# Kernel tuning notes

Measured on AMD Instinct MI355X. Metric: run time of the kernel, lower is better.

Reference implementation:

```python
import jax, jax.numpy as jnp
import numpy as np

B, T, C = 2, 2048, 2048
H, H_KV, D = 32, 8, 64
ROPE_THETA = 10000.0


def _rope_cos_sin(t, head_dim, theta=ROPE_THETA):
    # t: [T] positions. Returns interleaved cos/sin of shape [T, head_dim]
    inv_freq = 1.0 / theta ** (jnp.arange(0, head_dim, 2, dtype=jnp.float32) / head_dim)
    freqs = jnp.outer(t.astype(jnp.float32), inv_freq)  # [T, D/2]
    cos = jnp.stack([jnp.cos(freqs), jnp.cos(freqs)], axis=-1).reshape(t.shape[0], head_dim)
    sin = jnp.stack([jnp.sin(freqs), jnp.sin(freqs)], axis=-1).reshape(t.shape[0], head_dim)
    return cos[None, None], sin[None, None]  # [1,1,T,D]


def _rotate_half(x):
    half = x.shape[-1] // 2
    return jnp.concatenate([-x[..., half:], x[..., :half]], axis=-1)


def setup_inputs() -> dict:
    key = jax.random.key(0)
    ks = jax.random.split(key, 5)
    std = 0.02
    return {
        "x": jax.random.normal(ks[0], (B, T, C), dtype=jnp.float32),
        "Wq": jax.random.normal(ks[1], (H * D, C), dtype=jnp.float32) * std,
        "Wk": jax.random.normal(ks[2], (H_KV * D, C), dtype=jnp.float32) * std,
        "Wv": jax.random.normal(ks[3], (H_KV * D, C), dtype=jnp.float32) * std,
        "Wc": jax.random.normal(ks[4], (C, C), dtype=jnp.float32) * std,
        "position_ids": jnp.arange(T, dtype=jnp.int32)[None, :],  # [1, T]
    }


def reference(x, Wq, Wk, Wv, Wc, position_ids):
    b, t, c = x.shape
    # QKV projections (torch Linear: y = x @ W.T)
    q = (x @ Wq.T).reshape(b, t, H, D).transpose(0, 2, 1, 3)       # [B,H,T,D]
    k = (x @ Wk.T).reshape(b, t, H_KV, D).transpose(0, 2, 1, 3)    # [B,Hkv,T,D]
    v = (x @ Wv.T).reshape(b, t, H_KV, D).transpose(0, 2, 1, 3)
    # GQA expand: repeat_interleave along head dim
    rep = H // H_KV
    k = jnp.repeat(k, rep, axis=1)  # [B,H,T,D]
    v = jnp.repeat(v, rep, axis=1)
    # RoPE (single-batch branch: interleaved cos/sin)
    cos, sin = _rope_cos_sin(position_ids[0], D)
    q = q * cos + _rotate_half(q) * sin
    k = k * cos + _rotate_half(k) * sin
    # causal SDPA
    scale = 1.0 / jnp.sqrt(jnp.asarray(D, dtype=q.dtype))
    scores = jnp.einsum("bhqd,bhkd->bhqk", q, k) * scale
    causal = jnp.tril(jnp.ones((t, t), dtype=bool))
    scores = jnp.where(causal[None, None], scores, jnp.finfo(scores.dtype).min)
    attn = jax.nn.softmax(scores, axis=-1)
    y = jnp.einsum("bhqk,bhkd->bhqd", attn, v)  # [B,H,T,D]
    y = y.transpose(0, 2, 1, 3).reshape(b, t, c)
    return y @ Wc.T
```

## Files before the change

kernel.cpp:

```cpp
#include <hip/hip_runtime.h>

constexpr int B   = 2;
constexpr int T   = 2048;
constexpr int C   = 2048;
constexpr int H   = 32;
constexpr int HKV = 8;
constexpr int D   = 64;
constexpr float SCALE = 0.125f;

typedef __attribute__((ext_vector_type(8))) short bf16x8;
typedef __attribute__((ext_vector_type(4))) float f32x4;

__device__ __forceinline__ unsigned short f2bf(float f) {
    unsigned u = __builtin_bit_cast(unsigned, f);
    u += 0x7fff + ((u >> 16) & 1);
    return (unsigned short)(u >> 16);
}
__device__ __forceinline__ float bf2f(unsigned short u) {
    unsigned v = (unsigned)u << 16;
    return __builtin_bit_cast(float, v);
}
__device__ __forceinline__ unsigned cvt_pk_bf16(float lo, float hi) {
    unsigned r;
    asm("v_cvt_pk_bf16_f32 %0, %1, %2" : "=v"(r) : "v"(lo), "v"(hi));
    return r;
}

typedef __attribute__((address_space(1))) const unsigned char ga_t;
typedef __attribute__((address_space(3))) unsigned char lds_t;
__device__ __forceinline__ void gl2lds16(const void* g, void* l) {
    __builtin_amdgcn_global_load_lds((ga_t*)g, (lds_t*)l, 16, 0, 0);
}

__global__ __launch_bounds__(256) void cast_all_bf16(const float* __restrict__ x,
                                                     const float* __restrict__ wq,
                                                     const float* __restrict__ wk,
                                                     const float* __restrict__ wv,
                                                     const float* __restrict__ wc,
                                                     unsigned short* __restrict__ out) {
    const size_t b0 = (size_t)B * T * C;
    const size_t b1 = b0 + (size_t)H * D * C;
    const size_t b2 = b1 + (size_t)HKV * D * C;
    const size_t b3 = b2 + (size_t)HKV * D * C;
    size_t i = ((size_t)blockIdx.x * 256 + threadIdx.x) * 8;
    const float* src;
    size_t off;
    if (i < b0)      { src = x;  off = i; }
    else if (i < b1) { src = wq; off = i - b0; }
    else if (i < b2) { src = wk; off = i - b1; }
    else if (i < b3) { src = wv; off = i - b2; }
    else             { src = wc; off = i - b3; }
    float4 a = *(const float4*)(src + off);
    float4 b = *(const float4*)(src + off + 4);
    uint4 r;
    r.x = (unsigned)f2bf(a.x) | ((unsigned)f2bf(a.y) << 16);
    r.y = (unsigned)f2bf(a.z) | ((unsigned)f2bf(a.w) << 16);
    r.z = (unsigned)f2bf(b.x) | ((unsigned)f2bf(b.y) << 16);
    r.w = (unsigned)f2bf(b.z) | ((unsigned)f2bf(b.w) << 16);
    *(uint4*)(out + i) = r;
}

template <typename OutT>
__device__ __forceinline__ void gemm_mfma_body(const unsigned short* __restrict__ Xh,
                                               const unsigned short* __restrict__ Wh,
                                               OutT* __restrict__ Y,
                                               int Nloc, int K, int bm, int bn) {
    __shared__ __align__(16) unsigned short As[128 * 32];
    __shared__ __align__(16) unsigned short Bs[128 * 32];
    char* AsB = (char*)As;
    char* BsB = (char*)Bs;

    const int tid  = threadIdx.x;
    const int wave = tid >> 6, lane = tid & 63;
    const int wm = (wave >> 1) * 64, wn = (wave & 1) * 64;
    const int m = lane & 15, quad = lane >> 4;

    const int r0 = tid >> 2;
    const int cs = tid & 3;
    const int cg = cs ^ (r0 & 3);
    const int wbase = (tid & 192) * 16;

    const unsigned short* gA = Xh + (size_t)(bm + r0) * K + cg * 8;
    const unsigned short* gB = Wh + (size_t)(bn + r0) * K + cg * 8;
    const size_t rowStep64 = (size_t)64 * K;

    int aoff[4], boff[4];
#pragma unroll
    for (int mt = 0; mt < 4; ++mt) {
        int ra = wm + mt * 16 + m;
        aoff[mt] = ra * 64 + ((quad ^ (ra & 3)) * 16);
        int rb = wn + mt * 16 + m;
        boff[mt] = rb * 64 + ((quad ^ (rb & 3)) * 16);
    }

    f32x4 acc[4][4];
#pragma unroll
    for (int i = 0; i < 4; ++i)
#pragma unroll
        for (int j = 0; j < 4; ++j) acc[i][j] = (f32x4){0.f, 0.f, 0.f, 0.f};

    for (int k0 = 0; k0 < K; k0 += 32) {
        gl2lds16(gA,             AsB + wbase);
        gl2lds16(gA + rowStep64, AsB + 4096 + wbase);
        gl2lds16(gB,             BsB + wbase);
        gl2lds16(gB + rowStep64, BsB + 4096 + wbase);
        gA += 32;
        gB += 32;
        __syncthreads();

        bf16x8 af[4], bfr[4];
#pragma unroll
        for (int mt = 0; mt < 4; ++mt) af[mt]  = *(const bf16x8*)(AsB + aoff[mt]);
#pragma unroll
        for (int nt = 0; nt < 4; ++nt) bfr[nt] = *(const bf16x8*)(BsB + boff[nt]);
#pragma unroll
        for (int mt = 0; mt < 4; ++mt)
#pragma unroll
            for (int nt = 0; nt < 4; ++nt)
                acc[mt][nt] = __builtin_amdgcn_mfma_f32_16x16x32_bf16(af[mt], bfr[nt],
                                                                      acc[mt][nt], 0, 0, 0);
        __syncthreads();
    }

#pragma unroll
    for (int mt = 0; mt < 4; ++mt)
#pragma unroll
        for (int r = 0; r < 4; ++r) {
            size_t row = (size_t)(bm + wm + mt * 16 + quad * 4 + r);
#pragma unroll
            for (int nt = 0; nt < 4; ++nt) {
                int col = bn + wn + nt * 16 + m;
                float v = acc[mt][nt][r];
                if constexpr (sizeof(OutT) == 2)
                    Y[row * Nloc + col] = f2bf(v);
                else
                    Y[row * Nloc + col] = v;
            }
        }
}

__global__ __launch_bounds__(256) void qkv_gemm_bf16(const unsigned short* __restrict__ Xh,
                                                     const unsigned short* __restrict__ Wqh,
                                                     const unsigned short* __restrict__ Wkh,
                                                     const unsigned short* __restrict__ Wvh,
                                                     unsigned short* __restrict__ qh,
                                                     unsigned short* __restrict__ kh,
                                                     unsigned short* __restrict__ vh) {
    int bn0 = blockIdx.x * 128;
    const unsigned short* Wsel;
    unsigned short* Ysel;
    int bnl, Nloc;
    if (bn0 < H * D)                { Wsel = Wqh; Ysel = qh; bnl = bn0;                  Nloc = H * D;   }
    else if (bn0 < H*D + HKV*D)     { Wsel = Wkh; Ysel = kh; bnl = bn0 - H * D;          Nloc = HKV * D; }
    else                            { Wsel = Wvh; Ysel = vh; bnl = bn0 - H*D - HKV*D;    Nloc = HKV * D; }
    gemm_mfma_body<unsigned short>(Xh, Wsel, Ysel, Nloc, C, blockIdx.y * 128, bnl);
}

__global__ __launch_bounds__(256) void out_gemm_bf16(const unsigned short* __restrict__ Xh,
                                                     const unsigned short* __restrict__ Wh,
                                                     float* __restrict__ Y) {
    gemm_mfma_body<float>(Xh, Wh, Y, C, C, blockIdx.y * 128, blockIdx.x * 128);
}

__global__ void rope_fused(unsigned short* __restrict__ qh, unsigned short* __restrict__ kh,
                           const int* __restrict__ pos_ids, float qscale) {
    int idx = blockIdx.x * blockDim.x + threadIdx.x;
    const int qtotal = B * T * H * 32;
    unsigned short* buf;
    int nheads, rel;
    float sc;
    if (idx < qtotal) { buf = qh; nheads = H;   sc = qscale; rel = idx; }
    else              { buf = kh; nheads = HKV; sc = 1.0f;   rel = idx - qtotal; }
    int d = rel & 31;
    int rest = rel >> 5;
    int t = (rest / nheads) % T;
    float pos = (float)pos_ids[t];
    int i1 = d >> 1;
    const float NEG_LF = -(2.0f / 64.0f) * 13.287712379549449f;
    float a1 = pos * exp2f(NEG_LF * (float)i1);
    float a2 = pos * exp2f(NEG_LF * (float)(i1 + 16));
    float c1 = cosf(a1), s1 = sinf(a1);
    float c2 = cosf(a2), s2 = sinf(a2);
    size_t base = (size_t)rest * D + d;
    float x1 = bf2f(buf[base]), x2 = bf2f(buf[base + 32]);
    buf[base]      = f2bf((x1 * c1 - x2 * s1) * sc);
    buf[base + 32] = f2bf((x2 * c2 + x1 * s2) * sc);
}

__global__ __launch_bounds__(256) void v_transpose(const unsigned short* __restrict__ vh,
                                                   unsigned short* __restrict__ vtg) {
    __shared__ unsigned short Vs[64][72];
    const int t0 = blockIdx.x * 64;
    const int hkv = blockIdx.y;
    const int b = blockIdx.z;
    const int tid = threadIdx.x;

    for (int e = tid; e < 512; e += 256) {
        int t = e >> 3, d8 = (e & 7) * 8;
        uint4 val = *(const uint4*)(vh + ((size_t)((b * T + t0 + t) * HKV) + hkv) * D + d8);
        unsigned short tmp[8];
        *(uint4*)tmp = val;
#pragma unroll
        for (int i = 0; i < 8; ++i) Vs[d8 + i][t] = tmp[i];
    }
    __syncthreads();
    for (int e = tid; e < 512; e += 256) {
        int d = e >> 3, c = e & 7;
        *(uint4*)(vtg + ((size_t)((b * HKV + hkv) * D) + d) * T + t0 + c * 8) =
            *(const uint4*)&Vs[d][c * 8];
    }
}

__global__ __launch_bounds__(256, 6) void flash_attn_mfma(const unsigned short* __restrict__ Qh,
                                                          const unsigned short* __restrict__ Kh,
                                                          const unsigned short* __restrict__ Vtg,
                                                          unsigned short* __restrict__ Yh) {
    __shared__ __align__(16) unsigned short Ks[64 * 64];
    __shared__ __align__(16) unsigned short Vt[64 * 64];
    __shared__ __align__(16) unsigned short Ps[4][16][72];

    const int q0 = ((int)gridDim.x - 1 - (int)blockIdx.x) * 64;
    const int h  = blockIdx.y;
    const int b  = blockIdx.z;
    const int hkv = h >> 2;
    const int tid = threadIdx.x;
    const int wave = tid >> 6;
    const int lane = tid & 63;
    const int m = lane & 15;
    const int quad = lane >> 4;

    const unsigned short* qrow = Qh + ((size_t)((b * T + q0 + wave * 16 + m) * H) + h) * D;
    const bf16x8 qa0 = *(const bf16x8*)(qrow + quad * 8);
    const bf16x8 qa1 = *(const bf16x8*)(qrow + 32 + quad * 8);

    f32x4 o[4];
#pragma unroll
    for (int dt = 0; dt < 4; ++dt) o[dt] = (f32x4){0.f, 0.f, 0.f, 0.f};
    float ms = -1e30f, ls = 0.f;

    const int r0 = tid >> 3, cs = tid & 7, cg = cs ^ (r0 & 7);
    const int wbase = (tid & 192) * 16;
    const unsigned short* gK = Kh + ((size_t)(b * T) * HKV + hkv) * D
                                  + (size_t)r0 * (HKV * D) + cg * 8;
    const unsigned short* gV = Vtg + ((size_t)(b * HKV + hkv) * D) * (size_t)T
                                   + (size_t)r0 * T + cg * 8;
    char* KsB = (char*)Ks;
    char* VtB = (char*)Vt;

    const int qmin = q0 + wave * 16;

    for (int k0 = 0; k0 <= q0; k0 += 64) {
        gl2lds16(gK,                          KsB + wbase);
        gl2lds16(gK + (size_t)32 * (HKV * D), KsB + 4096 + wbase);
        gl2lds16(gV,                          VtB + wbase);
        gl2lds16(gV + (size_t)32 * T,         VtB + 4096 + wbase);
        gK += (size_t)64 * (HKV * D);
        gV += 64;
        __syncthreads();

        f32x4 s[4];
        __builtin_amdgcn_s_setprio(1);
#pragma unroll
        for (int nt = 0; nt < 4; ++nt) {
            const int kmin = k0 + nt * 16;
            if (kmin > qmin + 15) {
                s[nt] = (f32x4){-1e30f, -1e30f, -1e30f, -1e30f};
                continue;
            }
            int row = nt * 16 + m;
            const bf16x8 ka0 = *(const bf16x8*)(KsB + row * 128 + ((quad ^ (m & 7)) * 16));
            const bf16x8 ka1 = *(const bf16x8*)(KsB + row * 128 + (((quad + 4) ^ (m & 7)) * 16));
            f32x4 acc = (f32x4){0.f, 0.f, 0.f, 0.f};
            acc = __builtin_amdgcn_mfma_f32_16x16x32_bf16(ka0, qa0, acc, 0, 0, 0);
            acc = __builtin_amdgcn_mfma_f32_16x16x32_bf16(ka1, qa1, acc, 0, 0, 0);
            if (kmin + 15 > qmin) {
                int c0 = qmin - kmin + m - 4 * quad;
#pragma unroll
                for (int r = 0; r < 4; ++r)
                    if (r > c0) acc[r] = -1e30f;
            }
            s[nt] = acc;
        }
        __builtin_amdgcn_s_setprio(0);

        float mx = s[0][0];
#pragma unroll
        for (int nt = 0; nt < 4; ++nt)
#pragma unroll
            for (int r = 0; r < 4; ++r) mx = fmaxf(mx, s[nt][r]);
        mx = fmaxf(mx, __shfl_xor(mx, 16));
        mx = fmaxf(mx, __shfl_xor(mx, 32));

        float al = 1.0f;
        if (__any(mx > ms + 8.0f)) {
            float mnew = fmaxf(ms, mx);
            al = exp2f(ms - mnew);
            ms = mnew;
            float av[4];
#pragma unroll
            for (int r = 0; r < 4; ++r)
                av[r] = __shfl(al, quad * 20 + r);
#pragma unroll
            for (int dt = 0; dt < 4; ++dt)
#pragma unroll
                for (int r = 0; r < 4; ++r) o[dt][r] *= av[r];
        }

        float psum = 0.f;
#pragma unroll
        for (int nt = 0; nt < 4; ++nt) {
            float p0 = exp2f(s[nt][0] - ms);
            float p1 = exp2f(s[nt][1] - ms);
            float p2 = exp2f(s[nt][2] - ms);
            float p3 = exp2f(s[nt][3] - ms);
            psum += (p0 + p1) + (p2 + p3);
            uint2 w;
            w.x = cvt_pk_bf16(p0, p1);
            w.y = cvt_pk_bf16(p2, p3);
            *(uint2*)&Ps[wave][m][nt * 16 + quad * 4] = w;
        }
        psum += __shfl_xor(psum, 16);
        psum += __shfl_xor(psum, 32);
        ls = ls * al + psum;

        const bf16x8 pa0 = *(const bf16x8*)&Ps[wave][m][quad * 8];
        const bf16x8 pa1 = *(const bf16x8*)&Ps[wave][m][32 + quad * 8];
        __builtin_amdgcn_s_setprio(1);
#pragma unroll
        for (int dt = 0; dt < 4; ++dt) {
            int vrow = dt * 16 + m;
            const bf16x8 vb0 = *(const bf16x8*)(VtB + vrow * 128 + ((quad ^ (m & 7)) * 16));
            const bf16x8 vb1 = *(const bf16x8*)(VtB + vrow * 128 + (((quad + 4) ^ (m & 7)) * 16));
            o[dt] = __builtin_amdgcn_mfma_f32_16x16x32_bf16(pa0, vb0, o[dt], 0, 0, 0);
            o[dt] = __builtin_amdgcn_mfma_f32_16x16x32_bf16(pa1, vb1, o[dt], 0, 0, 0);
        }
        __builtin_amdgcn_s_setprio(0);
        __syncthreads();
    }

#pragma unroll
    for (int r = 0; r < 4; ++r) {
        float lv = __shfl(ls, quad * 20 + r);
        float inv = 1.0f / lv;
        int trow = q0 + wave * 16 + quad * 4 + r;
        unsigned short* yp = Yh + ((size_t)(b * T + trow) * H + h) * D;
#pragma unroll
        for (int dt = 0; dt < 4; ++dt)
            yp[dt * 16 + m] = f2bf(o[dt][r] * inv);
    }
}

extern "C" void kernel_launch(void* const* d_in, const int* in_sizes, int n_in,
                              void* d_out, int out_size, void* d_ws, size_t ws_size,
                              hipStream_t stream) {
    const float* x  = (const float*)d_in[0];
    const float* Wq = (const float*)d_in[1];
    const float* Wk = (const float*)d_in[2];
    const float* Wv = (const float*)d_in[3];
    const float* Wc = (const float*)d_in[4];
    const int*  pos = (const int*)d_in[5];
    float* out = (float*)d_out;

    unsigned short* xh  = (unsigned short*)d_ws;
    unsigned short* wqh = xh  + (size_t)B * T * C;
    unsigned short* wkh = wqh + (size_t)H * D * C;
    unsigned short* wvh = wkh + (size_t)HKV * D * C;
    unsigned short* wch = wvh + (size_t)HKV * D * C;
    unsigned short* qh  = wch + (size_t)C * C;
    unsigned short* kh  = qh  + (size_t)B * T * H * D;
    unsigned short* vh  = kh  + (size_t)B * T * HKV * D;
    unsigned short* vtg = vh  + (size_t)B * T * HKV * D;
    unsigned short* yh  = xh;

    const size_t cast_total = (size_t)B * T * C + (size_t)(H + 2 * HKV) * D * C + (size_t)C * C;
    cast_all_bf16<<<(unsigned)(cast_total / (256 * 8)), 256, 0, stream>>>(x, Wq, Wk, Wv, Wc, xh);

    dim3 g1((H * D + 2 * HKV * D) / 128, (B * T) / 128);
    qkv_gemm_bf16<<<g1, 256, 0, stream>>>(xh, wqh, wkh, wvh, qh, kh, vh);

    const float QSCALE = SCALE * 1.4426950408889634f;
    rope_fused<<<(B * T * (H + HKV) * 32) / 256, 256, 0, stream>>>(qh, kh, pos, QSCALE);
    v_transpose<<<dim3(T / 64, HKV, B), 256, 0, stream>>>(vh, vtg);

    dim3 g2(T / 64, H, B);
    flash_attn_mfma<<<g2, 256, 0, stream>>>(qh, kh, vtg, yh);

    dim3 g3(C / 128, (B * T) / 128);
    out_gemm_bf16<<<g3, 256, 0, stream>>>(yh, wch, out);
}
```

Measured before the change: 376.7 us.

## Prefetch next K/V tile into registers to overlap global loads with compute

Replaces the direct global-to-LDS loads in the attention loop with register staging. The next K/V tile is loaded into registers while the current tile is being computed, then written to LDS at the start of the following iteration. The __syncthreads calls become explicit lgkmcnt waits plus s_barrier, so the barrier no longer waits on outstanding global loads. This hides global load latency at the cost of extra VGPRs and explicit LDS store instructions, which may reduce occupancy.

```diff
diff --git a/kernel.cpp b/kernel.cpp
--- a/kernel.cpp
+++ b/kernel.cpp
@@ -239,7 +239,6 @@
     float ms = -1e30f, ls = 0.f;
 
     const int r0 = tid >> 3, cs = tid & 7, cg = cs ^ (r0 & 7);
-    const int wbase = (tid & 192) * 16;
     const unsigned short* gK = Kh + ((size_t)(b * T) * HKV + hkv) * D
                                   + (size_t)r0 * (HKV * D) + cg * 8;
     const unsigned short* gV = Vtg + ((size_t)(b * HKV + hkv) * D) * (size_t)T
@@ -249,14 +248,30 @@
 
     const int qmin = q0 + wave * 16;
 
+    uint4 rK0 = *(const uint4*)gK;
+    uint4 rK1 = *(const uint4*)(gK + (size_t)32 * (HKV * D));
+    uint4 rV0 = *(const uint4*)gV;
+    uint4 rV1 = *(const uint4*)(gV + (size_t)32 * T);
+    gK += (size_t)64 * (HKV * D);
+    gV += 64;
+
     for (int k0 = 0; k0 <= q0; k0 += 64) {
-        gl2lds16(gK,                          KsB + wbase);
-        gl2lds16(gK + (size_t)32 * (HKV * D), KsB + 4096 + wbase);
-        gl2lds16(gV,                          VtB + wbase);
-        gl2lds16(gV + (size_t)32 * T,         VtB + 4096 + wbase);
-        gK += (size_t)64 * (HKV * D);
-        gV += 64;
-        __syncthreads();
+        *(uint4*)(KsB + tid * 16)        = rK0;
+        *(uint4*)(KsB + 4096 + tid * 16) = rK1;
+        *(uint4*)(VtB + tid * 16)        = rV0;
+        *(uint4*)(VtB + 4096 + tid * 16) = rV1;
+        if (k0 + 64 <= q0) {
+            rK0 = *(const uint4*)gK;
+            rK1 = *(const uint4*)(gK + (size_t)32 * (HKV * D));
+            rV0 = *(const uint4*)gV;
+            rV1 = *(const uint4*)(gV + (size_t)32 * T);
+            gK += (size_t)64 * (HKV * D);
+            gV += 64;
+        }
+        __builtin_amdgcn_sched_barrier(0);
+        asm volatile("s_waitcnt lgkmcnt(0)" ::: "memory");
+        __builtin_amdgcn_s_barrier();
+        __builtin_amdgcn_sched_barrier(0);
 
         f32x4 s[4];
         __builtin_amdgcn_s_setprio(1);
@@ -335,7 +350,10 @@
             o[dt] = __builtin_amdgcn_mfma_f32_16x16x32_bf16(pa1, vb1, o[dt], 0, 0, 0);
         }
         __builtin_amdgcn_s_setprio(0);
-        __syncthreads();
+
+        asm volatile("s_waitcnt lgkmcnt(0)" ::: "memory");
+        __builtin_amdgcn_s_barrier();
+        __builtin_amdgcn_sched_barrier(0);
     }
 
 #pragma unroll
```

New measurement: 398.9 us. 5.9% more time.
